# Kernel optimization log

Hardware: AMD Instinct MI355X
Metric: run time of the kernel (lower is better)

Reference implementation:

```python
import jax, jax.numpy as jnp
import numpy as np

EPS = 1e-5

def _gather_particles(x, idx):
    # x: [B, C, M], idx: [B, N] -> [B, C, N]
    return jax.vmap(lambda a, i: a[:, i])(x, idx)

def _group_norm_dense(x, gamma, beta):
    # groups == channels (default GroupNorm(num_groups=out_channels)) -> per-channel over spatial
    m = x.mean(axis=(2, 3, 4), keepdims=True)
    v = x.var(axis=(2, 3, 4), keepdims=True)
    return (x - m) * jax.lax.rsqrt(v + EPS) * gamma[None, :, None, None, None] + beta[None, :, None, None, None]

def _group_norm_particles(x, gamma, beta):
    # x: [B, C, N]; per-channel norm over particle dim
    m = x.mean(axis=2, keepdims=True)
    v = x.var(axis=2, keepdims=True)
    return (x - m) * jax.lax.rsqrt(v + EPS) * gamma[None, :, None] + beta[None, :, None]

def _apr_conv(x, w, neighbor_idx):
    # x: [B, Cin, N]; w: [Cout, Cin, K]; neighbor_idx: [B, N, K]
    K = w.shape[2]
    out = jnp.zeros((x.shape[0], w.shape[0], x.shape[2]), x.dtype)
    for k in range(K):  # small fixed stencil
        xg = _gather_particles(x, neighbor_idx[:, :, k])  # [B, Cin, N]
        out = out + jnp.einsum('bcn,oc->bon', xg, w[:, :, k])
    return out

def setup_inputs() -> dict:
    key = jax.random.key(0)
    ks = jax.random.split(key, 12)
    B, Cin, D = 2, 64, 40
    Nc, Nf, K = 100_000, 400_000, 7
    Ch = Cin // 2  # 32
    Cout = 32
    S = D * D * D
    return {
        'x1': jax.random.normal(ks[0], (B, Cin, D, D, D), jnp.float32),
        'x2': jax.random.normal(ks[1], (B, Ch, Nf), jnp.float32),
        'w_reduce': jax.random.normal(ks[2], (Ch, Cin), jnp.float32) * 0.1,
        'gnr_gamma': jnp.ones((Ch,), jnp.float32),
        'gnr_beta': jnp.zeros((Ch,), jnp.float32),
        'w1': jax.random.normal(ks[3], (Cout, Cin, K), jnp.float32) * 0.1,
        'g1': jnp.ones((Cout,), jnp.float32),
        'b1': jnp.zeros((Cout,), jnp.float32),
        'w2': jax.random.normal(ks[4], (Cout, Cout, K), jnp.float32) * 0.1,
        'g2': jnp.ones((Cout,), jnp.float32),
        'b2': jnp.zeros((Cout,), jnp.float32),
        'sample_idx': jax.random.randint(ks[5], (B, Nc), 0, S, jnp.int32),
        'upsample_idx': jax.random.randint(ks[6], (B, Nf), 0, Nc, jnp.int32),
        'neighbor_idx': jax.random.randint(ks[7], (B, Nf, K), 0, Nf, jnp.int32),
    }

def reference(x1, x2, w_reduce, gnr_gamma, gnr_beta, w1, g1, b1, w2, g2, b2, sample_idx, upsample_idx, neighbor_idx):
    # reduce_ch: 1x1x1 conv (no bias) + GroupNorm + ReLU
    y = jnp.einsum('bcdhw,oc->bodhw', x1, w_reduce)
    y = jax.nn.relu(_group_norm_dense(y, gnr_gamma, gnr_beta))
    B, C = y.shape[0], y.shape[1]
    yf = y.reshape(B, C, -1)  # [B, C, S]
    # SampleParticles: dense voxel -> coarse particle gather
    coarse = _gather_particles(yf, sample_idx)  # [B, C, Nc]
    # UpSampleConst: coarse particle -> fine particle constant replication
    fine = _gather_particles(coarse, upsample_idx)  # [B, C, Nf]
    x = jnp.concatenate([x2, fine], axis=1)  # [B, 2C, Nf]
    # ConvBlock: two APR stencil conv + GroupNorm + ReLU blocks
    h = jax.nn.relu(_group_norm_particles(_apr_conv(x, w1, neighbor_idx), g1, b1))
    h = jax.nn.relu(_group_norm_particles(_apr_conv(h, w2, neighbor_idx), g2, b2))
    return h
```

## Files before the change

### kernel.cpp

```cpp
#include <hip/hip_runtime.h>
#include <cstdint>


typedef unsigned short u16;
typedef u16 u16x8 __attribute__((ext_vector_type(8)));
typedef float f4 __attribute__((ext_vector_type(4)));
using s16x8 = __attribute__((ext_vector_type(8))) short;
using u16x4 = __attribute__((ext_vector_type(4))) u16;

#define EPS 1e-5f
#define BB 2
#define CIN 64
#define CH 32
#define SVOX 64000
#define NC 100000
#define NF 400000

static __device__ __forceinline__ float b2f(u16 h) {
    return __builtin_bit_cast(float, (unsigned)h << 16);
}
static __device__ __forceinline__ u16 f2b(float f) {
    unsigned u = __builtin_bit_cast(unsigned, f);
    u += 0x7FFFu + ((u >> 16) & 1u);
    return (u16)(u >> 16);
}
static __device__ __forceinline__ f4 mfma16(s16x8 a, s16x8 b, f4 c) {
    return __builtin_amdgcn_mfma_f32_16x16x32_bf16(a, b, c, 0, 0, 0);
}

__global__ __launch_bounds__(256) void k_prep(
    const float* __restrict__ w1, const float* __restrict__ w2,
    float* __restrict__ stats, u16* __restrict__ wf1, u16* __restrict__ wf2)
{
    int t0 = blockIdx.x * 256 + threadIdx.x, stride = gridDim.x * 256;
    for (int i = t0; i < 12288; i += stride) stats[i] = 0.f;
    for (int i = t0; i < 14 * 2 * 512; i += stride) {
        int j = i & 7, l = (i >> 3) & 63, ot = (i >> 9) & 1, s = i >> 10;
        int k = s >> 1, h = s & 1;
        int c = h * 32 + (l >> 4) * 8 + j;
        int o = ot * 16 + (l & 15);
        wf1[i] = f2b(w1[(o * CIN + c) * 7 + k]);
    }
    for (int i = t0; i < 7 * 2 * 512; i += stride) {
        int j = i & 7, l = (i >> 3) & 63, ot = (i >> 9) & 1, k = i >> 10;
        int c = (l >> 4) * 8 + j;
        int o = ot * 16 + (l & 15);
        wf2[i] = f2b(w2[(o * CH + c) * 7 + k]);
    }
}

__global__ __launch_bounds__(256) void k_reduce(
    const float* __restrict__ x1, const float* __restrict__ wr,
    u16* __restrict__ y, float* __restrict__ statsA)
{
    __shared__ float wl[CIN * CH];
    __shared__ float sred[64];
    int tid = threadIdx.x, b = blockIdx.y;
    if (tid < 64) sred[tid] = 0.f;
    for (int i = tid; i < CIN * CH; i += 256) {
        int c = i >> 5, o = i & 31;
        wl[i] = wr[o * CIN + c];
    }
    __syncthreads();
    int s0 = blockIdx.x * 512 + tid;
    int s1 = s0 + 256;
    const float* xb = x1 + (size_t)b * CIN * SVOX;
    float acc0[CH], acc1[CH];
#pragma unroll
    for (int o = 0; o < CH; o++) { acc0[o] = 0.f; acc1[o] = 0.f; }
    for (int c = 0; c < CIN; c++) {
        float xv0 = __builtin_nontemporal_load(&xb[(size_t)c * SVOX + s0]);
        float xv1 = __builtin_nontemporal_load(&xb[(size_t)c * SVOX + s1]);
        const float* w = &wl[c * CH];
#pragma unroll
        for (int o = 0; o < CH; o++) {
            float wv = w[o];
            acc0[o] = fmaf(xv0, wv, acc0[o]);
            acc1[o] = fmaf(xv1, wv, acc1[o]);
        }
    }
    u16* y0 = y + ((size_t)b * SVOX + s0) * CH;
    u16* y1 = y + ((size_t)b * SVOX + s1) * CH;
#pragma unroll
    for (int g = 0; g < 4; g++) {
        u16x8 v0, v1;
#pragma unroll
        for (int i = 0; i < 8; i++) {
            v0[i] = f2b(acc0[g * 8 + i]);
            v1[i] = f2b(acc1[g * 8 + i]);
        }
        ((u16x8*)y0)[g] = v0;
        ((u16x8*)y1)[g] = v1;
    }
    int lane = tid & 63;
#pragma unroll
    for (int g = 0; g < 4; g++) {
        float s[8], qq[8];
#pragma unroll
        for (int i = 0; i < 8; i++) {
            int o = g * 8 + i;
            s[i] = acc0[o] + acc1[o];
            qq[i] = fmaf(acc0[o], acc0[o], acc1[o] * acc1[o]);
        }
#pragma unroll
        for (int m = 1; m < 64; m <<= 1) {
#pragma unroll
            for (int i = 0; i < 8; i++) {
                s[i] += __shfl_xor(s[i], m);
                qq[i] += __shfl_xor(qq[i], m);
            }
        }
        if (lane == 0) {
#pragma unroll
            for (int i = 0; i < 8; i++) {
                atomicAdd(&sred[(g * 8 + i) * 2], s[i]);
                atomicAdd(&sred[(g * 8 + i) * 2 + 1], qq[i]);
            }
        }
    }
    __syncthreads();
    if (tid < 64) atomicAdd(&statsA[(size_t)(b * 64 + tid) * 32], sred[tid]);
}

__global__ __launch_bounds__(256) void k_build(
    const float* __restrict__ x2, const u16* __restrict__ y,
    const float* __restrict__ statsA, const float* __restrict__ gA,
    const float* __restrict__ bA, const int* __restrict__ sidx,
    const int* __restrict__ uidx, u16* __restrict__ comb)
{
    __shared__ u16 tile[64][40];
    __shared__ float sl[CH * 2];
    int tid = threadIdx.x, b = blockIdx.y;
    if (tid < CH) {
        float sum = statsA[(size_t)(b * 64 + tid * 2) * 32];
        float sq  = statsA[(size_t)(b * 64 + tid * 2 + 1) * 32];
        float mean = sum * (1.f / SVOX);
        float var = sq * (1.f / SVOX) - mean * mean;
        float sc = rsqrtf(var + EPS) * gA[tid];
        sl[tid * 2] = sc;
        sl[tid * 2 + 1] = bA[tid] - mean * sc;
    }
    int c = tid >> 3, no = (tid & 7) * 8;
    int nl = tid >> 3, seg = tid & 7;
    for (int t = blockIdx.x; t < 6250; t += gridDim.x) {
        int n0 = t * 64;
        const float* src = x2 + ((size_t)b * CH + c) * NF + n0 + no;
        f4 v0 = __builtin_nontemporal_load((const f4*)src);
        f4 v1 = __builtin_nontemporal_load((const f4*)(src + 4));
        __syncthreads();
#pragma unroll
        for (int i = 0; i < 4; i++) tile[no + i][c] = f2b(v0[i]);
#pragma unroll
        for (int i = 0; i < 4; i++) tile[no + 4 + i][c] = f2b(v1[i]);
        __syncthreads();
#pragma unroll
        for (int it = 0; it < 2; it++) {
            int n = n0 + it * 32 + nl;
            u16x8 ov;
            if (seg < 4) {
                int co = seg * 8;
#pragma unroll
                for (int i = 0; i < 8; i++) ov[i] = tile[it * 32 + nl][co + i];
            } else {
                int u = uidx[(size_t)b * NF + n];
                int j = sidx[(size_t)b * NC + u];
                const u16x8* yr = (const u16x8*)(y + ((size_t)b * SVOX + j) * CH);
                u16x8 v = yr[seg - 4];
                int co = (seg - 4) * 8;
#pragma unroll
                for (int i = 0; i < 8; i++)
                    ov[i] = f2b(fmaxf(fmaf(b2f(v[i]), sl[(co + i) * 2], sl[(co + i) * 2 + 1]), 0.f));
            }
            *(u16x8*)(comb + ((size_t)b * NF + n) * 64 + seg * 8) = ov;
        }
    }
}

__global__ __launch_bounds__(512) void k_conv1(
    const u16* __restrict__ comb, const u16* __restrict__ wfg,
    const int* __restrict__ nbr, u16* __restrict__ h1,
    float* __restrict__ stats1)
{
    __shared__ u16 wf[14 * 2 * 512];
    __shared__ float sst[64];
    int tid = threadIdx.x, b = blockIdx.y;
    if (tid < 64) sst[tid] = 0.f;
    const f4* wsrc = (const f4*)wfg;
    f4* wdst = (f4*)wf;
    for (int i = tid; i < 1792; i += 512) wdst[i] = wsrc[i];
    __syncthreads();
    const s16x8* wfv = (const s16x8*)wf;
    int lane = tid & 63, wave = tid >> 6;
    int p = lane & 15, q = lane >> 4;
    int n = blockIdx.x * 128 + wave * 16 + p;
    const u16* Cb = comb + (size_t)b * NF * 64;
    const int* nbb = nbr + ((size_t)b * NF + n) * 7;
    int i0[7];
#pragma unroll
    for (int k = 0; k < 7; k++) i0[k] = __builtin_nontemporal_load(&nbb[k]);
    s16x8 rlo[7], rhi[7];
#pragma unroll
    for (int k = 0; k < 7; k++) {
        const u16* rec = Cb + (size_t)i0[k] * 64;
        rlo[k] = __builtin_bit_cast(s16x8, *(const u16x8*)(rec + q * 8));
        rhi[k] = __builtin_bit_cast(s16x8, *(const u16x8*)(rec + 32 + q * 8));
    }
    f4 acc0 = {0.f, 0.f, 0.f, 0.f};
    f4 acc1 = {0.f, 0.f, 0.f, 0.f};
#pragma unroll
    for (int k = 0; k < 7; k++) {
        acc0 = mfma16(wfv[(k * 4 + 0) * 64 + lane], rlo[k], acc0);
        acc1 = mfma16(wfv[(k * 4 + 1) * 64 + lane], rlo[k], acc1);
        acc0 = mfma16(wfv[(k * 4 + 2) * 64 + lane], rhi[k], acc0);
        acc1 = mfma16(wfv[(k * 4 + 3) * 64 + lane], rhi[k], acc1);
    }
    float s[8], t[8];
#pragma unroll
    for (int r = 0; r < 4; r++) {
        s[r] = acc0[r];     t[r] = acc0[r] * acc0[r];
        s[4 + r] = acc1[r]; t[4 + r] = acc1[r] * acc1[r];
    }
#pragma unroll
    for (int m = 1; m < 16; m <<= 1) {
#pragma unroll
        for (int j = 0; j < 8; j++) {
            s[j] += __shfl_xor(s[j], m);
            t[j] += __shfl_xor(t[j], m);
        }
    }
    if (p == 0) {
#pragma unroll
        for (int r = 0; r < 4; r++) {
            atomicAdd(&sst[(q * 4 + r) * 2],       s[r]);
            atomicAdd(&sst[(q * 4 + r) * 2 + 1],   t[r]);
            atomicAdd(&sst[(16 + q * 4 + r) * 2],     s[4 + r]);
            atomicAdd(&sst[(16 + q * 4 + r) * 2 + 1], t[4 + r]);
        }
    }
    u16x4 v0, v1;
#pragma unroll
    for (int r = 0; r < 4; r++) { v0[r] = f2b(acc0[r]); v1[r] = f2b(acc1[r]); }
    u16* out = h1 + ((size_t)b * NF + n) * CH + q * 4;
    __builtin_nontemporal_store(v0, (u16x4*)out);
    __builtin_nontemporal_store(v1, (u16x4*)(out + 16));
    __syncthreads();
    if (tid < 64) atomicAdd(&stats1[(size_t)(b * 64 + tid) * 32], sst[tid]);
}

__global__ __launch_bounds__(512) void k_conv2(
    const u16* __restrict__ x, const u16* __restrict__ wfg,
    const int* __restrict__ nbr, const float* __restrict__ stats1,
    const float* __restrict__ g1, const float* __restrict__ b1,
    float* __restrict__ out, float* __restrict__ stats2)
{
    __shared__ u16 wf[7 * 2 * 512];
    __shared__ float sst[64];
    int tid = threadIdx.x, b = blockIdx.y;
    if (tid < 64) sst[tid] = 0.f;
    const f4* wsrc = (const f4*)wfg;
    f4* wdst = (f4*)wf;
    for (int i = tid; i < 896; i += 512) wdst[i] = wsrc[i];
    __syncthreads();
    const s16x8* wfv = (const s16x8*)wf;
    int lane = tid & 63, wave = tid >> 6;
    int p = lane & 15, q = lane >> 4;
    int n = blockIdx.x * 128 + wave * 16 + p;
    const u16* Xb = x + (size_t)b * NF * CH;
    const int* nbb = nbr + ((size_t)b * NF + n) * 7;
    int i0[7];
#pragma unroll
    for (int k = 0; k < 7; k++) i0[k] = __builtin_nontemporal_load(&nbb[k]);
    float sc[8], sh[8];
#pragma unroll
    for (int j = 0; j < 8; j++) {
        int ch = q * 8 + j;
        float sum = stats1[(size_t)(b * 64 + ch * 2) * 32];
        float sq  = stats1[(size_t)(b * 64 + ch * 2 + 1) * 32];
        float mean = sum * (1.f / NF);
        float var = sq * (1.f / NF) - mean * mean;
        float s = rsqrtf(var + EPS) * g1[ch];
        sc[j] = s;
        sh[j] = b1[ch] - mean * s;
    }
    u16x8 raw[7];
#pragma unroll
    for (int k = 0; k < 7; k++)
        raw[k] = *(const u16x8*)(Xb + (size_t)i0[k] * CH + q * 8);
    f4 acc0 = {0.f, 0.f, 0.f, 0.f};
    f4 acc1 = {0.f, 0.f, 0.f, 0.f};
#pragma unroll
    for (int k = 0; k < 7; k++) {
        u16x8 nv;
#pragma unroll
        for (int j = 0; j < 8; j++)
            nv[j] = f2b(fmaxf(fmaf(b2f(raw[k][j]), sc[j], sh[j]), 0.f));
        s16x8 a = __builtin_bit_cast(s16x8, nv);
        acc0 = mfma16(wfv[(k * 2 + 0) * 64 + lane], a, acc0);
        acc1 = mfma16(wfv[(k * 2 + 1) * 64 + lane], a, acc1);
    }
    float s[8], t[8];
#pragma unroll
    for (int r = 0; r < 4; r++) {
        s[r] = acc0[r];     t[r] = acc0[r] * acc0[r];
        s[4 + r] = acc1[r]; t[4 + r] = acc1[r] * acc1[r];
    }
#pragma unroll
    for (int m = 1; m < 16; m <<= 1) {
#pragma unroll
        for (int j = 0; j < 8; j++) {
            s[j] += __shfl_xor(s[j], m);
            t[j] += __shfl_xor(t[j], m);
        }
    }
    if (p == 0) {
#pragma unroll
        for (int r = 0; r < 4; r++) {
            atomicAdd(&sst[(q * 4 + r) * 2],       s[r]);
            atomicAdd(&sst[(q * 4 + r) * 2 + 1],   t[r]);
            atomicAdd(&sst[(16 + q * 4 + r) * 2],     s[4 + r]);
            atomicAdd(&sst[(16 + q * 4 + r) * 2 + 1], t[4 + r]);
        }
    }
    float* ob = out + (size_t)b * CH * NF + n;
#pragma unroll
    for (int r = 0; r < 4; r++) {
        __builtin_nontemporal_store(acc0[r], &ob[(size_t)(q * 4 + r) * NF]);
        __builtin_nontemporal_store(acc1[r], &ob[(size_t)(16 + q * 4 + r) * NF]);
    }
    __syncthreads();
    if (tid < 64) atomicAdd(&stats2[(size_t)(b * 64 + tid) * 32], sst[tid]);
}

__global__ __launch_bounds__(256) void k_norm2c(
    float* __restrict__ h, const float* __restrict__ stats2,
    const float* __restrict__ g2, const float* __restrict__ b2)
{
    const int total = BB * CH * (NF / 4);
    for (int i4 = blockIdx.x * 256 + threadIdx.x; i4 < total; i4 += gridDim.x * 256) {
        int cf = i4 / (NF / 4);
        int o = cf & 31;
        float sum = stats2[(size_t)(cf * 2) * 32];
        float sq  = stats2[(size_t)(cf * 2 + 1) * 32];
        float mean = sum * (1.f / NF);
        float var = sq * (1.f / NF) - mean * mean;
        float sc = rsqrtf(var + EPS) * g2[o];
        float sh = b2[o] - mean * sc;
        f4 v = __builtin_nontemporal_load(&((f4*)h)[i4]);
#pragma unroll
        for (int j = 0; j < 4; j++) v[j] = fmaxf(fmaf(v[j], sc, sh), 0.f);
        __builtin_nontemporal_store(v, &((f4*)h)[i4]);
    }
}

extern "C" void kernel_launch(void* const* d_in, const int* in_sizes, int n_in,
                              void* d_out, int out_size, void* d_ws, size_t ws_size,
                              hipStream_t stream)
{
    const float* x1 = (const float*)d_in[0];
    const float* x2 = (const float*)d_in[1];
    const float* wr = (const float*)d_in[2];
    const float* gA = (const float*)d_in[3];
    const float* bA = (const float*)d_in[4];
    const float* w1 = (const float*)d_in[5];
    const float* g1 = (const float*)d_in[6];
    const float* b1 = (const float*)d_in[7];
    const float* w2 = (const float*)d_in[8];
    const float* g2 = (const float*)d_in[9];
    const float* b2 = (const float*)d_in[10];
    const int* sidx = (const int*)d_in[11];
    const int* uidx = (const int*)d_in[12];
    const int* nbr  = (const int*)d_in[13];

    char* ws = (char*)d_ws;
    u16* h1      = (u16*)ws;
    u16* y       = (u16*)(ws + 51200000);
    float* stats = (float*)(ws + 59392000);
    float* statsA = stats;
    float* stats1 = (float*)(ws + 59392000 + 16384);
    float* stats2 = (float*)(ws + 59392000 + 32768);
    u16* wf1g = (u16*)(ws + 59392000 + 49152);
    u16* wf2g = (u16*)(ws + 59392000 + 49152 + 28672);
    u16* comb = (u16*)d_out;

    k_prep<<<48, 256, 0, stream>>>(w1, w2, stats, wf1g, wf2g);
    k_reduce<<<dim3(125, BB), 256, 0, stream>>>(x1, wr, y, statsA);
    k_build<<<dim3(1024, BB), 256, 0, stream>>>(x2, y, statsA, gA, bA, sidx, uidx, comb);
    k_conv1<<<dim3(3125, BB), 512, 0, stream>>>(comb, wf1g, nbr, h1, stats1);
    k_conv2<<<dim3(3125, BB), 512, 0, stream>>>(h1, wf2g, nbr, stats1, g1, b1, (float*)d_out, stats2);
    k_norm2c<<<2048, 256, 0, stream>>>((float*)d_out, stats2, g2, b2);
}
```

Before: 545.3 us.

## Process batches sequentially per launch and drop nontemporal hints to keep data cache-resident

The build, conv1 and conv2 kernels now run in a host loop, one batch per launch, instead of covering both batches in a single 2D grid. Each gather stage then works on a single batch's comb or h1 buffer, which halves the working set that random neighbor gathers touch. Nontemporal loads and stores on h1 and the output are replaced with ordinary accesses, so freshly written data can stay in cache for the next kernel. The cost is extra kernel launches and less parallelism per launch. Regular stores may also evict other useful lines.

Result: slower. 565.6 us (+3.7%).

```diff
diff --git a/kernel.cpp b/kernel.cpp
--- a/kernel.cpp
+++ b/kernel.cpp
@@ -126,11 +126,11 @@
     const float* __restrict__ x2, const u16* __restrict__ y,
     const float* __restrict__ statsA, const float* __restrict__ gA,
     const float* __restrict__ bA, const int* __restrict__ sidx,
-    const int* __restrict__ uidx, u16* __restrict__ comb)
+    const int* __restrict__ uidx, u16* __restrict__ comb, int b)
 {
     __shared__ u16 tile[64][40];
     __shared__ float sl[CH * 2];
-    int tid = threadIdx.x, b = blockIdx.y;
+    int tid = threadIdx.x;
     if (tid < CH) {
         float sum = statsA[(size_t)(b * 64 + tid * 2) * 32];
         float sq  = statsA[(size_t)(b * 64 + tid * 2 + 1) * 32];
@@ -179,11 +179,11 @@
 __global__ __launch_bounds__(512) void k_conv1(
     const u16* __restrict__ comb, const u16* __restrict__ wfg,
     const int* __restrict__ nbr, u16* __restrict__ h1,
-    float* __restrict__ stats1)
+    float* __restrict__ stats1, int b)
 {
     __shared__ u16 wf[14 * 2 * 512];
     __shared__ float sst[64];
-    int tid = threadIdx.x, b = blockIdx.y;
+    int tid = threadIdx.x;
     if (tid < 64) sst[tid] = 0.f;
     const f4* wsrc = (const f4*)wfg;
     f4* wdst = (f4*)wf;
@@ -241,8 +241,8 @@
 #pragma unroll
     for (int r = 0; r < 4; r++) { v0[r] = f2b(acc0[r]); v1[r] = f2b(acc1[r]); }
     u16* out = h1 + ((size_t)b * NF + n) * CH + q * 4;
-    __builtin_nontemporal_store(v0, (u16x4*)out);
-    __builtin_nontemporal_store(v1, (u16x4*)(out + 16));
+    *(u16x4*)out = v0;
+    *(u16x4*)(out + 16) = v1;
     __syncthreads();
     if (tid < 64) atomicAdd(&stats1[(size_t)(b * 64 + tid) * 32], sst[tid]);
 }
@@ -251,11 +251,11 @@
     const u16* __restrict__ x, const u16* __restrict__ wfg,
     const int* __restrict__ nbr, const float* __restrict__ stats1,
     const float* __restrict__ g1, const float* __restrict__ b1,
-    float* __restrict__ out, float* __restrict__ stats2)
+    float* __restrict__ out, float* __restrict__ stats2, int b)
 {
     __shared__ u16 wf[7 * 2 * 512];
     __shared__ float sst[64];
-    int tid = threadIdx.x, b = blockIdx.y;
+    int tid = threadIdx.x;
     if (tid < 64) sst[tid] = 0.f;
     const f4* wsrc = (const f4*)wfg;
     f4* wdst = (f4*)wf;
@@ -324,8 +324,8 @@
     float* ob = out + (size_t)b * CH * NF + n;
 #pragma unroll
     for (int r = 0; r < 4; r++) {
-        __builtin_nontemporal_store(acc0[r], &ob[(size_t)(q * 4 + r) * NF]);
-        __builtin_nontemporal_store(acc1[r], &ob[(size_t)(16 + q * 4 + r) * NF]);
+        ob[(size_t)(q * 4 + r) * NF] = acc0[r];
+        ob[(size_t)(16 + q * 4 + r) * NF] = acc1[r];
     }
     __syncthreads();
     if (tid < 64) atomicAdd(&stats2[(size_t)(b * 64 + tid) * 32], sst[tid]);
@@ -345,10 +345,10 @@
         float var = sq * (1.f / NF) - mean * mean;
         float sc = rsqrtf(var + EPS) * g2[o];
         float sh = b2[o] - mean * sc;
-        f4 v = __builtin_nontemporal_load(&((f4*)h)[i4]);
+        f4 v = ((f4*)h)[i4];
 #pragma unroll
         for (int j = 0; j < 4; j++) v[j] = fmaxf(fmaf(v[j], sc, sh), 0.f);
-        __builtin_nontemporal_store(v, &((f4*)h)[i4]);
+        ((f4*)h)[i4] = v;
     }
 }
 
@@ -384,8 +384,10 @@
 
     k_prep<<<48, 256, 0, stream>>>(w1, w2, stats, wf1g, wf2g);
     k_reduce<<<dim3(125, BB), 256, 0, stream>>>(x1, wr, y, statsA);
-    k_build<<<dim3(1024, BB), 256, 0, stream>>>(x2, y, statsA, gA, bA, sidx, uidx, comb);
-    k_conv1<<<dim3(3125, BB), 512, 0, stream>>>(comb, wf1g, nbr, h1, stats1);
-    k_conv2<<<dim3(3125, BB), 512, 0, stream>>>(h1, wf2g, nbr, stats1, g1, b1, (float*)d_out, stats2);
+    for (int b = 0; b < BB; b++) {
+        k_build<<<1024, 256, 0, stream>>>(x2, y, statsA, gA, bA, sidx, uidx, comb, b);
+        k_conv1<<<3125, 512, 0, stream>>>(comb, wf1g, nbr, h1, stats1, b);
+        k_conv2<<<3125, 512, 0, stream>>>(h1, wf2g, nbr, stats1, g1, b1, (float*)d_out, stats2, b);
+    }
     k_norm2c<<<2048, 256, 0, stream>>>((float*)d_out, stats2, g2, b2);
 }
```

## Store conv2 output as bf16 point-major and transpose during final norm

Applied to the files above, without the earlier changes.

conv2 now writes bf16 in point-major layout to scratch buffers, split per batch into separate launches, instead of fp32 channel-major strided stores into the output. The final norm kernel reads the bf16 tile, applies GroupNorm+ReLU, transposes through shared memory and writes coalesced fp32 output. Nontemporal stores in conv1 become plain stores. This halves intermediate traffic and makes conv2's stores contiguous, at the cost of bf16 rounding of pre-norm activations and extra launches.

New measurement: 538.3 us. Within noise of the previous version (-1.3%).

```diff
diff --git a/kernel.cpp b/kernel.cpp
--- a/kernel.cpp
+++ b/kernel.cpp
@@ -241,8 +241,8 @@
 #pragma unroll
     for (int r = 0; r < 4; r++) { v0[r] = f2b(acc0[r]); v1[r] = f2b(acc1[r]); }
     u16* out = h1 + ((size_t)b * NF + n) * CH + q * 4;
-    __builtin_nontemporal_store(v0, (u16x4*)out);
-    __builtin_nontemporal_store(v1, (u16x4*)(out + 16));
+    *(u16x4*)out = v0;
+    *(u16x4*)(out + 16) = v1;
     __syncthreads();
     if (tid < 64) atomicAdd(&stats1[(size_t)(b * 64 + tid) * 32], sst[tid]);
 }
@@ -251,11 +251,11 @@
     const u16* __restrict__ x, const u16* __restrict__ wfg,
     const int* __restrict__ nbr, const float* __restrict__ stats1,
     const float* __restrict__ g1, const float* __restrict__ b1,
-    float* __restrict__ out, float* __restrict__ stats2)
+    u16* __restrict__ h2, float* __restrict__ stats2, int b)
 {
     __shared__ u16 wf[7 * 2 * 512];
     __shared__ float sst[64];
-    int tid = threadIdx.x, b = blockIdx.y;
+    int tid = threadIdx.x;
     if (tid < 64) sst[tid] = 0.f;
     const f4* wsrc = (const f4*)wfg;
     f4* wdst = (f4*)wf;
@@ -321,34 +321,52 @@
             atomicAdd(&sst[(16 + q * 4 + r) * 2 + 1], t[4 + r]);
         }
     }
-    float* ob = out + (size_t)b * CH * NF + n;
-#pragma unroll
-    for (int r = 0; r < 4; r++) {
-        __builtin_nontemporal_store(acc0[r], &ob[(size_t)(q * 4 + r) * NF]);
-        __builtin_nontemporal_store(acc1[r], &ob[(size_t)(16 + q * 4 + r) * NF]);
-    }
+    u16x4 v0, v1;
+#pragma unroll
+    for (int r = 0; r < 4; r++) { v0[r] = f2b(acc0[r]); v1[r] = f2b(acc1[r]); }
+    u16* outp = h2 + (size_t)n * CH + q * 4;
+    *(u16x4*)outp = v0;
+    *(u16x4*)(outp + 16) = v1;
     __syncthreads();
     if (tid < 64) atomicAdd(&stats2[(size_t)(b * 64 + tid) * 32], sst[tid]);
 }
 
-__global__ __launch_bounds__(256) void k_norm2c(
-    float* __restrict__ h, const float* __restrict__ stats2,
-    const float* __restrict__ g2, const float* __restrict__ b2)
-{
-    const int total = BB * CH * (NF / 4);
-    for (int i4 = blockIdx.x * 256 + threadIdx.x; i4 < total; i4 += gridDim.x * 256) {
-        int cf = i4 / (NF / 4);
-        int o = cf & 31;
-        float sum = stats2[(size_t)(cf * 2) * 32];
-        float sq  = stats2[(size_t)(cf * 2 + 1) * 32];
+__global__ __launch_bounds__(256) void k_norm2t(
+    const u16* __restrict__ h2, const float* __restrict__ stats2,
+    const float* __restrict__ g2, const float* __restrict__ b2,
+    float* __restrict__ out, int b)
+{
+    __shared__ float sl[64];
+    __shared__ float tile[CH][72];
+    int tid = threadIdx.x;
+    if (tid < CH) {
+        float sum = stats2[(size_t)(b * 64 + tid * 2) * 32];
+        float sq  = stats2[(size_t)(b * 64 + tid * 2 + 1) * 32];
         float mean = sum * (1.f / NF);
         float var = sq * (1.f / NF) - mean * mean;
-        float sc = rsqrtf(var + EPS) * g2[o];
-        float sh = b2[o] - mean * sc;
-        f4 v = __builtin_nontemporal_load(&((f4*)h)[i4]);
-#pragma unroll
-        for (int j = 0; j < 4; j++) v[j] = fmaxf(fmaf(v[j], sc, sh), 0.f);
-        __builtin_nontemporal_store(v, &((f4*)h)[i4]);
+        float sc = rsqrtf(var + EPS) * g2[tid];
+        sl[tid * 2] = sc;
+        sl[tid * 2 + 1] = b2[tid] - mean * sc;
+    }
+    int p = tid >> 2, c0 = (tid & 3) * 8;
+    int c = tid >> 3, p0 = (tid & 7) * 8;
+    float* ob = out + (size_t)b * CH * NF;
+    for (int t = blockIdx.x; t < 6250; t += gridDim.x) {
+        int n0 = t * 64;
+        u16x8 v = *(const u16x8*)(h2 + (size_t)(n0 + p) * CH + c0);
+        __syncthreads();
+#pragma unroll
+        for (int i = 0; i < 8; i++) {
+            int cc = c0 + i;
+            tile[cc][p] = fmaxf(fmaf(b2f(v[i]), sl[cc * 2], sl[cc * 2 + 1]), 0.f);
+        }
+        __syncthreads();
+        f4 o0, o1;
+#pragma unroll
+        for (int i = 0; i < 4; i++) { o0[i] = tile[c][p0 + i]; o1[i] = tile[c][p0 + 4 + i]; }
+        float* dst = ob + (size_t)c * NF + n0 + p0;
+        *(f4*)dst = o0;
+        *(f4*)(dst + 4) = o1;
     }
 }
 
@@ -380,12 +398,16 @@
     float* stats2 = (float*)(ws + 59392000 + 32768);
     u16* wf1g = (u16*)(ws + 59392000 + 49152);
     u16* wf2g = (u16*)(ws + 59392000 + 49152 + 28672);
-    u16* comb = (u16*)d_out;
+    u16* comb  = (u16*)d_out;
+    u16* h2b0  = (u16*)((char*)d_out + 76800000);
+    u16* h2b1  = (u16*)ws;
 
     k_prep<<<48, 256, 0, stream>>>(w1, w2, stats, wf1g, wf2g);
     k_reduce<<<dim3(125, BB), 256, 0, stream>>>(x1, wr, y, statsA);
     k_build<<<dim3(1024, BB), 256, 0, stream>>>(x2, y, statsA, gA, bA, sidx, uidx, comb);
     k_conv1<<<dim3(3125, BB), 512, 0, stream>>>(comb, wf1g, nbr, h1, stats1);
-    k_conv2<<<dim3(3125, BB), 512, 0, stream>>>(h1, wf2g, nbr, stats1, g1, b1, (float*)d_out, stats2);
-    k_norm2c<<<2048, 256, 0, stream>>>((float*)d_out, stats2, g2, b2);
-}
+    k_conv2<<<3125, 512, 0, stream>>>(h1, wf2g, nbr, stats1, g1, b1, h2b0, stats2, 0);
+    k_conv2<<<3125, 512, 0, stream>>>(h1, wf2g, nbr, stats1, g1, b1, h2b1, stats2, 1);
+    k_norm2t<<<2048, 256, 0, stream>>>(h2b0, stats2, g2, b2, (float*)d_out, 0);
+    k_norm2t<<<2048, 256, 0, stream>>>(h2b1, stats2, g2, b2, (float*)d_out, 1);
+}
```
